# Performance work log

Measured on AMD Instinct MI355X. Metric: run time of the kernel, lower is better.

The kernel has to match this reference:

```python
import jax, jax.numpy as jnp
import numpy as np
from jax import lax


def _conv(x, w, b):
    # NCHW x OIHW, stride 1, VALID padding (matches nn.Conv2d padding=0)
    y = lax.conv_general_dilated(x, w, (1, 1), 'VALID',
                                 dimension_numbers=('NCHW', 'OIHW', 'NCHW'))
    return y + b[None, :, None, None]


def _maxpool2(x):
    return lax.reduce_window(x, -jnp.inf, lax.max, (1, 1, 2, 2), (1, 1, 2, 2), 'VALID')


def setup_inputs() -> dict:
    key = jax.random.key(0)
    ks = jax.random.split(key, 8)
    B, C, H, W = 4096, 3, 32, 32
    E, NC = 8, 1000  # out_dim (=n learners), num_classes
    inp = {
        'x': jax.random.normal(ks[0], (B, C, H, W), jnp.float32),
        'conv1_w': jax.random.normal(ks[1], (1, 3, 5, 5), jnp.float32) * 0.1,
        'conv1_b': jnp.zeros((1,), jnp.float32),
        'conv2_w': jax.random.normal(ks[2], (2, 1, 5, 5), jnp.float32) * 0.1,
        'conv2_b': jnp.zeros((2,), jnp.float32),
        'conv3_w': jax.random.normal(ks[3], (4, 2, 5, 5), jnp.float32) * 0.1,
        'conv3_b': jnp.zeros((4,), jnp.float32),
        'fc_w': jax.random.normal(ks[4], (E, 4), jnp.float32) * 0.5,
        'fc_b': jnp.zeros((E,), jnp.float32),
        'ens_w': jax.random.normal(ks[5], (E, C * H * W, NC), jnp.float32) * 0.02,
        'ens_b': jnp.zeros((E, NC), jnp.float32),
        'k': 2,
    }
    return inp


def reference(x, conv1_w, conv1_b, conv2_w, conv2_b, conv3_w, conv3_b,
              fc_w, fc_b, ens_w, ens_b, k):
    B = x.shape[0]
    # --- selector CNN stem ---
    h = jax.nn.relu(_conv(x, conv1_w, conv1_b))   # [B,1,28,28]
    h = _maxpool2(h)                              # [B,1,14,14]
    h = jax.nn.relu(_conv(h, conv2_w, conv2_b))   # [B,2,10,10]
    h = _maxpool2(h)                              # [B,2,5,5]
    h = jax.nn.relu(_conv(h, conv3_w, conv3_b))   # [B,4,1,1]
    h = h.reshape(B, -1)                          # [B,4]
    z = h @ fc_w.T + fc_b                         # [B,E]
    # L2NormalizationLayer with clamp(min=1e-9)
    z = z / jnp.clip(jnp.linalg.norm(z, axis=-1, keepdims=True), 1e-9, None)
    # TopK -> one-hot routing mask (straight-through style forward)
    _, idx = lax.top_k(z, k)                      # [B,k]
    mask = jax.nn.one_hot(idx, z.shape[-1], dtype=z.dtype).sum(-2)  # [B,E] in {0,1}
    # --- frozen ensemble: linear weak learners, combined via mask ---
    xf = x.reshape(B, -1)                          # [B,F]
    outs = jnp.einsum('bf,efc->bec', xf, ens_w) + ens_b[None]  # [B,E,NC]
    return (outs * mask[:, :, None]).sum(axis=1)   # [B,NC]
```

## Files before the change

kernel.cpp:

```cpp
#include <hip/hip_runtime.h>
#include <hip/hip_bf16.h>
#include <stdint.h>

#define B_SZ 4096
#define F_SZ 3072
#define NCLS 1000
#define NE 8
#define NPAD 1024
#define CAP 4096

#define OFF_CNT   0
#define OFF_LIST  1024
#define OFF_PAIR  132096
#define OFF_XB    262144
#define OFF_WT    25427968

typedef unsigned short u16;
typedef __attribute__((ext_vector_type(8))) short short8v;
typedef __attribute__((ext_vector_type(4))) float f32x4;

__device__ __forceinline__ u16 f2bf(float f) {
  unsigned int u = __float_as_uint(f);
  u = (u + 0x7FFFu + ((u >> 16) & 1u)) >> 16;
  return (u16)u;
}

__device__ __forceinline__ void gll16(const void* g, void* l) {
  __builtin_amdgcn_global_load_lds(
      (const __attribute__((address_space(1))) void*)g,
      (__attribute__((address_space(3))) void*)l, 16, 0, 0);
}

__global__ __launch_bounds__(256) void transpose_w(const float* __restrict__ ensw,
                                                   u16* __restrict__ wt) {
  __shared__ u16 tile[64 * 68];
  int t = threadIdx.x;
  int n0 = blockIdx.x * 64, k0 = blockIdx.y * 64, e = blockIdx.z;
  const float* src = ensw + (size_t)e * (F_SZ * NCLS);
  int kr = t >> 4, nq = (t & 15) * 4;
  for (int it = 0; it < 4; ++it) {
    int kk = kr + it * 16;
    const float* sp = src + (size_t)(k0 + kk) * NCLS + n0 + nq;
    float4 v;
    if (n0 + nq + 3 < NCLS) v = *(const float4*)sp;
    else {
      v.x = (n0 + nq     < NCLS) ? sp[0] : 0.f;
      v.y = (n0 + nq + 1 < NCLS) ? sp[1] : 0.f;
      v.z = (n0 + nq + 2 < NCLS) ? sp[2] : 0.f;
      v.w = (n0 + nq + 3 < NCLS) ? sp[3] : 0.f;
    }
    u16* d = tile + kk * 68 + nq;
    d[0] = f2bf(v.x); d[1] = f2bf(v.y); d[2] = f2bf(v.z); d[3] = f2bf(v.w);
  }
  __syncthreads();
  int rn = t >> 3, c8 = t & 7;
  for (int it = 0; it < 2; ++it) {
    int n = rn + it * 32;
    u16 o[8];
#pragma unroll
    for (int jj = 0; jj < 8; ++jj) o[jj] = tile[(c8 * 8 + jj) * 68 + n];
    uint4 pk;
    pk.x = (unsigned)o[0] | ((unsigned)o[1] << 16);
    pk.y = (unsigned)o[2] | ((unsigned)o[3] << 16);
    pk.z = (unsigned)o[4] | ((unsigned)o[5] << 16);
    pk.w = (unsigned)o[6] | ((unsigned)o[7] << 16);
    *(uint4*)(wt + ((size_t)(e * NPAD + n0 + n)) * F_SZ + k0 + c8 * 8) = pk;
  }
}

#define XST 36
#define XCH 1152
__global__ __launch_bounds__(128) void selector(
    const float* __restrict__ x,
    const float* __restrict__ w1, const float* __restrict__ b1,
    const float* __restrict__ w2, const float* __restrict__ b2,
    const float* __restrict__ w3, const float* __restrict__ b3,
    const float* __restrict__ fw, const float* __restrict__ fb,
    u16* __restrict__ xb16, int* __restrict__ cnt, int* __restrict__ list,
    int* __restrict__ expair) {
  __shared__ float wgt[384];
  __shared__ float S[2][4704];
  int t = threadIdx.x;
  for (int i = t; i < 372; i += 128) {
    float v;
    if      (i <  75) v = w1[i];
    else if (i <  76) v = b1[i - 75];
    else if (i < 126) v = w2[i - 76];
    else if (i < 128) v = b2[i - 126];
    else if (i < 328) v = w3[i - 128];
    else if (i < 332) v = b3[i - 328];
    else if (i < 364) v = fw[i - 332];
    else              v = fb[i - 364];
    wgt[i] = v;
  }
  int w = t >> 6, l = t & 63;
  int b = blockIdx.x * 2 + w;
  float* xs   = S[w];
  float* buf1 = xs + 3456;
  float* p1   = xs + 4240;
  float* buf2 = xs + 4436;
  float* p2   = xs + 4636;
  float* hb   = xs + 4686;
  float* zb   = xs + 4690;

  const float4* gx = (const float4*)(x + (size_t)b * F_SZ);
  ushort4* gxb = (ushort4*)(xb16 + (size_t)b * F_SZ);
  for (int it = 0; it < 12; ++it) {
    int idx = it * 64 + l;
    float4 v = gx[idx];
    int f = idx * 4;
    int c = f >> 10, rem = f & 1023, y = rem >> 5, xc = rem & 31;
    *(float4*)(xs + c * XCH + y * XST + xc) = v;
    ushort4 h4;
    h4.x = f2bf(v.x); h4.y = f2bf(v.y); h4.z = f2bf(v.z); h4.w = f2bf(v.w);
    gxb[idx] = h4;
  }
  __syncthreads();

  if (l < 56) {
    int y = l >> 1, xh = l & 1;
    float acc[14];
#pragma unroll
    for (int xc = 0; xc < 14; ++xc) acc[xc] = wgt[75];
    for (int c = 0; c < 3; ++c)
      for (int i = 0; i < 5; ++i) {
        const float4* rb = (const float4*)(xs + c * XCH + (y + i) * XST) + xh * 3;
        float a[20];
#pragma unroll
        for (int q = 0; q < 5; ++q) {
          float4 v = rb[q];
          a[q * 4] = v.x; a[q * 4 + 1] = v.y; a[q * 4 + 2] = v.z; a[q * 4 + 3] = v.w;
        }
        if (xh) {
#pragma unroll
          for (int q = 0; q < 18; ++q) a[q] = a[q + 2];
        }
        const float* wp = wgt + c * 25 + i * 5;
        float W0 = wp[0], W1 = wp[1], W2 = wp[2], W3 = wp[3], W4 = wp[4];
#pragma unroll
        for (int xc = 0; xc < 14; ++xc)
          acc[xc] += a[xc] * W0 + a[xc + 1] * W1 + a[xc + 2] * W2 + a[xc + 3] * W3 + a[xc + 4] * W4;
      }
#pragma unroll
    for (int xc = 0; xc < 14; ++xc) buf1[y * 28 + xh * 14 + xc] = fmaxf(acc[xc], 0.f);
  }
  __syncthreads();

  for (int it = 0; it < 4; ++it) {
    int p = it * 64 + l;
    if (p < 196) {
      int py = p / 14, px = p % 14;
      const float* r0 = buf1 + (2 * py) * 28 + 2 * px;
      p1[p] = fmaxf(fmaxf(r0[0], r0[1]), fmaxf(r0[28], r0[29]));
    }
  }
  __syncthreads();

  for (int it = 0; it < 4; ++it) {
    int p = it * 64 + l;
    if (p < 200) {
      int o = p / 100, rem = p % 100, yy = rem / 10, xx = rem % 10;
      float acc = wgt[126 + o];
      const float* wp = wgt + 76 + o * 25;
      for (int i = 0; i < 5; ++i)
#pragma unroll
        for (int j = 0; j < 5; ++j) acc += p1[(yy + i) * 14 + xx + j] * wp[i * 5 + j];
      buf2[p] = fmaxf(acc, 0.f);
    }
  }
  __syncthreads();

  if (l < 50) {
    int o = l / 25, rem = l % 25, yy = rem / 5, xx = rem % 5;
    const float* r0 = buf2 + o * 100 + (2 * yy) * 10 + 2 * xx;
    p2[l] = fmaxf(fmaxf(r0[0], r0[1]), fmaxf(r0[10], r0[11]));
  }
  __syncthreads();

  if (l < 4) {
    float acc = wgt[328 + l];
    const float* wp = wgt + 128 + l * 50;
    for (int cc = 0; cc < 50; ++cc) acc += p2[cc] * wp[cc];
    hb[l] = fmaxf(acc, 0.f);
  }
  __syncthreads();

  if (l < 8) {
    float acc = wgt[364 + l];
    const float* wp = wgt + 332 + l * 4;
#pragma unroll
    for (int j = 0; j < 4; ++j) acc += hb[j] * wp[j];
    zb[l] = acc;
  }
  __syncthreads();

  if (l == 0) {
    float zz[8];
#pragma unroll
    for (int e = 0; e < 8; ++e) zz[e] = zb[e];
    int e1 = 0; float v1 = zz[0];
    for (int e = 1; e < 8; ++e) if (zz[e] > v1) { v1 = zz[e]; e1 = e; }
    int e2 = -1; float v2 = 0.f;
    for (int e = 0; e < 8; ++e) {
      if (e == e1) continue;
      if (e2 < 0 || zz[e] > v2) { v2 = zz[e]; e2 = e; }
    }
    int p1i = atomicAdd(&cnt[e1], 1); list[e1 * CAP + p1i] = b;
    int p2i = atomicAdd(&cnt[e2], 1); list[e2 * CAP + p2i] = b;
    expair[b] = e1 | (e2 << 8);
  }
}

__global__ __launch_bounds__(256) void bias_init(const int* __restrict__ expair,
                                                 const float* __restrict__ ensb,
                                                 float* __restrict__ out) {
  int b = blockIdx.x;
  int t = threadIdx.x;
  if (t >= 250) return;
  int pr = expair[b];
  const float4* p1 = (const float4*)(ensb + (size_t)(pr & 255) * NCLS);
  const float4* p2 = (const float4*)(ensb + (size_t)((pr >> 8) & 255) * NCLS);
  float4* op = (float4*)(out + (size_t)b * NCLS);
  float4 a = p1[t], c = p2[t];
  float4 r; r.x = a.x + c.x; r.y = a.y + c.y; r.z = a.z + c.z; r.w = a.w + c.w;
  op[t] = r;
}

__global__ __launch_bounds__(256) void moe_gemm(const u16* __restrict__ xb,
                                                const u16* __restrict__ wt,
                                                const int* __restrict__ cnt,
                                                const int* __restrict__ list,
                                                float* __restrict__ out) {
  __shared__ u16 As[2][8192];
  __shared__ u16 Bs[2][8192];
  __shared__ int idx_s[128];
  int e = blockIdx.z;
  int cnt_e = cnt[e];
  int m0 = blockIdx.y * 128;
  if (m0 >= cnt_e) return;
  int n0 = blockIdx.x * 128;
  int t = threadIdx.x;
  const int* lst = list + e * CAP;
  if (t < 128) idx_s[t] = lst[min(m0 + t, cnt_e - 1)];
  __syncthreads();

  int tr = t >> 3;
  int ts = t & 7;
  int g  = ts ^ (tr & 7);
  const u16* pA[4]; const u16* pB[4]; int ldst[4];
#pragma unroll
  for (int q = 0; q < 4; ++q) {
    int row = q * 32 + tr;
    pA[q] = xb + (size_t)idx_s[row] * F_SZ + g * 8;
    pB[q] = wt + ((size_t)(e * NPAD + n0 + row)) * F_SZ + g * 8;
    ldst[q] = (q * 256 + t) * 8;
  }

  int w = t >> 6, l = t & 63;
  int lr = l & 15, hk = l >> 4;
  int wrow = (w >> 1) * 64, wcol = (w & 1) * 64;
  int rA[4], rB[4];
#pragma unroll
  for (int i = 0; i < 4; ++i) {
    rA[i] = (wrow + i * 16 + lr) * 64;
    rB[i] = (wcol + i * 16 + lr) * 64;
  }
  int sw0 = ((hk    ) ^ (lr & 7)) * 8;
  int sw1 = ((hk + 4) ^ (lr & 7)) * 8;

#pragma unroll
  for (int q = 0; q < 4; ++q) { gll16(pA[q], &As[0][ldst[q]]); pA[q] += 64; }
#pragma unroll
  for (int q = 0; q < 4; ++q) { gll16(pB[q], &Bs[0][ldst[q]]); pB[q] += 64; }
  __syncthreads();

  f32x4 acc[4][4] = {};
  for (int s = 0; s < 48; ++s) {
    int cur = s & 1;
    if (s < 47) {
      int nxt = cur ^ 1;
#pragma unroll
      for (int q = 0; q < 4; ++q) { gll16(pA[q], &As[nxt][ldst[q]]); pA[q] += 64; }
#pragma unroll
      for (int q = 0; q < 4; ++q) { gll16(pB[q], &Bs[nxt][ldst[q]]); pB[q] += 64; }
    }
    short8v av[2][4], bv[2][4];
#pragma unroll
    for (int i = 0; i < 4; ++i) {
      av[0][i] = *(const short8v*)(&As[cur][rA[i] + sw0]);
      av[1][i] = *(const short8v*)(&As[cur][rA[i] + sw1]);
      bv[0][i] = *(const short8v*)(&Bs[cur][rB[i] + sw0]);
      bv[1][i] = *(const short8v*)(&Bs[cur][rB[i] + sw1]);
    }
#pragma unroll
    for (int h = 0; h < 2; ++h)
#pragma unroll
      for (int i = 0; i < 4; ++i)
#pragma unroll
        for (int j = 0; j < 4; ++j)
          acc[i][j] = __builtin_amdgcn_mfma_f32_16x16x32_bf16(av[h][i], bv[h][j], acc[i][j], 0, 0, 0);
    __syncthreads();
  }

#pragma unroll
  for (int i = 0; i < 4; ++i) {
#pragma unroll
    for (int r = 0; r < 4; ++r) {
      int mt = wrow + i * 16 + hk * 4 + r;
      if (m0 + mt < cnt_e) {
        float* orow = out + (size_t)idx_s[mt] * NCLS;
#pragma unroll
        for (int j = 0; j < 4; ++j) {
          int col = n0 + wcol + j * 16 + lr;
          if (col < NCLS) unsafeAtomicAdd(orow + col, acc[i][j][r]);
        }
      }
    }
  }
}

extern "C" void kernel_launch(void* const* d_in, const int* in_sizes, int n_in,
                              void* d_out, int out_size, void* d_ws, size_t ws_size,
                              hipStream_t stream) {
  const float* x   = (const float*)d_in[0];
  const float* w1  = (const float*)d_in[1];
  const float* b1  = (const float*)d_in[2];
  const float* w2  = (const float*)d_in[3];
  const float* b2  = (const float*)d_in[4];
  const float* w3  = (const float*)d_in[5];
  const float* b3  = (const float*)d_in[6];
  const float* fw  = (const float*)d_in[7];
  const float* fb  = (const float*)d_in[8];
  const float* ensw = (const float*)d_in[9];
  const float* ensb = (const float*)d_in[10];
  float* out = (float*)d_out;

  uint8_t* ws = (uint8_t*)d_ws;
  int* cnt    = (int*)(ws + OFF_CNT);
  int* list   = (int*)(ws + OFF_LIST);
  int* expair = (int*)(ws + OFF_PAIR);
  u16* xb16   = (u16*)(ws + OFF_XB);
  u16* wt     = (u16*)(ws + OFF_WT);

  hipMemsetAsync(cnt, 0, 64, stream);
  transpose_w<<<dim3(16, 48, 8), 256, 0, stream>>>(ensw, wt);
  selector<<<2048, 128, 0, stream>>>(x, w1, b1, w2, b2, w3, b3, fw, fb,
                                     xb16, cnt, list, expair);
  bias_init<<<4096, 256, 0, stream>>>(expair, ensb, out);
  moe_gemm<<<dim3(8, 32, 8), 256, 0, stream>>>(xb16, wt, cnt, list, out);
}
```

Before: 483.2 us.

## Split MoE GEMM along K, single-buffer LDS, and widen weight transpose tiles

The MoE GEMM grid gains a split-K dimension of 2, with each half's partial sums combined through the existing atomic adds into the output. LDS double buffering is replaced by a single buffer with a sync before and after each reload, and a launch bound hint targets 4 blocks per CU. The aim is more parallelism and occupancy for an expert-routed GEMM whose per-expert M tiles can be few. The weight transpose kernel now handles 256-wide K tiles and writes transposed rows with vectorized LDS reads, and two selector loops are unrolled. The price is less load/compute overlap inside each block and twice the atomic traffic.

```diff
diff --git a/kernel.cpp b/kernel.cpp
--- a/kernel.cpp
+++ b/kernel.cpp
@@ -8,6 +8,8 @@
 #define NE 8
 #define NPAD 1024
 #define CAP 4096
+#define KSPLIT 2
+#define KCH (F_SZ / KSPLIT)
 
 #define OFF_CNT   0
 #define OFF_LIST  1024
@@ -33,38 +35,35 @@
 
 __global__ __launch_bounds__(256) void transpose_w(const float* __restrict__ ensw,
                                                    u16* __restrict__ wt) {
-  __shared__ u16 tile[64 * 68];
+  __shared__ u16 tile[64 * 264];
   int t = threadIdx.x;
-  int n0 = blockIdx.x * 64, k0 = blockIdx.y * 64, e = blockIdx.z;
+  int n0 = blockIdx.x * 64, k0 = blockIdx.y * 256, e = blockIdx.z;
   const float* src = ensw + (size_t)e * (F_SZ * NCLS);
   int kr = t >> 4, nq = (t & 15) * 4;
-  for (int it = 0; it < 4; ++it) {
-    int kk = kr + it * 16;
+  for (int it = 0; it < 16; ++it) {
+    int kk = it * 16 + kr;
     const float* sp = src + (size_t)(k0 + kk) * NCLS + n0 + nq;
-    float4 v;
-    if (n0 + nq + 3 < NCLS) v = *(const float4*)sp;
+    int n = n0 + nq;
+    float4 v = make_float4(0.f, 0.f, 0.f, 0.f);
+    if (n + 3 < NCLS) v = *(const float4*)sp;
     else {
-      v.x = (n0 + nq     < NCLS) ? sp[0] : 0.f;
-      v.y = (n0 + nq + 1 < NCLS) ? sp[1] : 0.f;
-      v.z = (n0 + nq + 2 < NCLS) ? sp[2] : 0.f;
-      v.w = (n0 + nq + 3 < NCLS) ? sp[3] : 0.f;
-    }
-    u16* d = tile + kk * 68 + nq;
-    d[0] = f2bf(v.x); d[1] = f2bf(v.y); d[2] = f2bf(v.z); d[3] = f2bf(v.w);
-  }
-  __syncthreads();
-  int rn = t >> 3, c8 = t & 7;
-  for (int it = 0; it < 2; ++it) {
-    int n = rn + it * 32;
-    u16 o[8];
-#pragma unroll
-    for (int jj = 0; jj < 8; ++jj) o[jj] = tile[(c8 * 8 + jj) * 68 + n];
-    uint4 pk;
-    pk.x = (unsigned)o[0] | ((unsigned)o[1] << 16);
-    pk.y = (unsigned)o[2] | ((unsigned)o[3] << 16);
-    pk.z = (unsigned)o[4] | ((unsigned)o[5] << 16);
-    pk.w = (unsigned)o[6] | ((unsigned)o[7] << 16);
-    *(uint4*)(wt + ((size_t)(e * NPAD + n0 + n)) * F_SZ + k0 + c8 * 8) = pk;
+      if (n     < NCLS) v.x = sp[0];
+      if (n + 1 < NCLS) v.y = sp[1];
+      if (n + 2 < NCLS) v.z = sp[2];
+      if (n + 3 < NCLS) v.w = sp[3];
+    }
+    u16* d = tile + nq * 264 + kk;
+    d[0]   = f2bf(v.x);
+    d[264] = f2bf(v.y);
+    d[528] = f2bf(v.z);
+    d[792] = f2bf(v.w);
+  }
+  __syncthreads();
+  int kc = t & 31, nr = t >> 5;
+  for (int it = 0; it < 8; ++it) {
+    int n = it * 8 + nr;
+    uint4 pk = *(const uint4*)(tile + n * 264 + kc * 8);
+    *(uint4*)(wt + ((size_t)(e * NPAD + n0 + n)) * F_SZ + k0 + kc * 8) = pk;
   }
 }
 
@@ -162,6 +161,7 @@
       int o = p / 100, rem = p % 100, yy = rem / 10, xx = rem % 10;
       float acc = wgt[126 + o];
       const float* wp = wgt + 76 + o * 25;
+#pragma unroll
       for (int i = 0; i < 5; ++i)
 #pragma unroll
         for (int j = 0; j < 5; ++j) acc += p1[(yy + i) * 14 + xx + j] * wp[i * 5 + j];
@@ -180,6 +180,7 @@
   if (l < 4) {
     float acc = wgt[328 + l];
     const float* wp = wgt + 128 + l * 50;
+#pragma unroll
     for (int cc = 0; cc < 50; ++cc) acc += p2[cc] * wp[cc];
     hb[l] = fmaxf(acc, 0.f);
   }
@@ -226,15 +227,15 @@
   op[t] = r;
 }
 
-__global__ __launch_bounds__(256) void moe_gemm(const u16* __restrict__ xb,
-                                                const u16* __restrict__ wt,
-                                                const int* __restrict__ cnt,
-                                                const int* __restrict__ list,
-                                                float* __restrict__ out) {
-  __shared__ u16 As[2][8192];
-  __shared__ u16 Bs[2][8192];
+__global__ __launch_bounds__(256, 4) void moe_gemm(const u16* __restrict__ xb,
+                                                   const u16* __restrict__ wt,
+                                                   const int* __restrict__ cnt,
+                                                   const int* __restrict__ list,
+                                                   float* __restrict__ out) {
+  __shared__ u16 As[8192];
+  __shared__ u16 Bs[8192];
   __shared__ int idx_s[128];
-  int e = blockIdx.z;
+  int e = blockIdx.z >> 1, ks = blockIdx.z & 1;
   int cnt_e = cnt[e];
   int m0 = blockIdx.y * 128;
   if (m0 >= cnt_e) return;
@@ -244,15 +245,14 @@
   if (t < 128) idx_s[t] = lst[min(m0 + t, cnt_e - 1)];
   __syncthreads();
 
-  int tr = t >> 3;
-  int ts = t & 7;
+  int tr = t >> 3, ts = t & 7;
   int g  = ts ^ (tr & 7);
   const u16* pA[4]; const u16* pB[4]; int ldst[4];
 #pragma unroll
   for (int q = 0; q < 4; ++q) {
     int row = q * 32 + tr;
-    pA[q] = xb + (size_t)idx_s[row] * F_SZ + g * 8;
-    pB[q] = wt + ((size_t)(e * NPAD + n0 + row)) * F_SZ + g * 8;
+    pA[q] = xb + (size_t)idx_s[row] * F_SZ + ks * KCH + g * 8;
+    pB[q] = wt + ((size_t)(e * NPAD + n0 + row)) * F_SZ + ks * KCH + g * 8;
     ldst[q] = (q * 256 + t) * 8;
   }
 
@@ -269,28 +269,20 @@
   int sw1 = ((hk + 4) ^ (lr & 7)) * 8;
 
 #pragma unroll
-  for (int q = 0; q < 4; ++q) { gll16(pA[q], &As[0][ldst[q]]); pA[q] += 64; }
-#pragma unroll
-  for (int q = 0; q < 4; ++q) { gll16(pB[q], &Bs[0][ldst[q]]); pB[q] += 64; }
-  __syncthreads();
+  for (int q = 0; q < 4; ++q) { gll16(pA[q], &As[ldst[q]]); pA[q] += 64; }
+#pragma unroll
+  for (int q = 0; q < 4; ++q) { gll16(pB[q], &Bs[ldst[q]]); pB[q] += 64; }
 
   f32x4 acc[4][4] = {};
-  for (int s = 0; s < 48; ++s) {
-    int cur = s & 1;
-    if (s < 47) {
-      int nxt = cur ^ 1;
-#pragma unroll
-      for (int q = 0; q < 4; ++q) { gll16(pA[q], &As[nxt][ldst[q]]); pA[q] += 64; }
-#pragma unroll
-      for (int q = 0; q < 4; ++q) { gll16(pB[q], &Bs[nxt][ldst[q]]); pB[q] += 64; }
-    }
+  for (int s = 0; s < KCH / 64; ++s) {
+    __syncthreads();
     short8v av[2][4], bv[2][4];
 #pragma unroll
     for (int i = 0; i < 4; ++i) {
-      av[0][i] = *(const short8v*)(&As[cur][rA[i] + sw0]);
-      av[1][i] = *(const short8v*)(&As[cur][rA[i] + sw1]);
-      bv[0][i] = *(const short8v*)(&Bs[cur][rB[i] + sw0]);
-      bv[1][i] = *(const short8v*)(&Bs[cur][rB[i] + sw1]);
+      av[0][i] = *(const short8v*)(&As[rA[i] + sw0]);
+      av[1][i] = *(const short8v*)(&As[rA[i] + sw1]);
+      bv[0][i] = *(const short8v*)(&Bs[rB[i] + sw0]);
+      bv[1][i] = *(const short8v*)(&Bs[rB[i] + sw1]);
     }
 #pragma unroll
     for (int h = 0; h < 2; ++h)
@@ -299,7 +291,13 @@
 #pragma unroll
         for (int j = 0; j < 4; ++j)
           acc[i][j] = __builtin_amdgcn_mfma_f32_16x16x32_bf16(av[h][i], bv[h][j], acc[i][j], 0, 0, 0);
-    __syncthreads();
+    if (s < KCH / 64 - 1) {
+      __syncthreads();
+#pragma unroll
+      for (int q = 0; q < 4; ++q) { gll16(pA[q], &As[ldst[q]]); pA[q] += 64; }
+#pragma unroll
+      for (int q = 0; q < 4; ++q) { gll16(pB[q], &Bs[ldst[q]]); pB[q] += 64; }
+    }
   }
 
 #pragma unroll
@@ -343,9 +341,9 @@
   u16* wt     = (u16*)(ws + OFF_WT);
 
   hipMemsetAsync(cnt, 0, 64, stream);
-  transpose_w<<<dim3(16, 48, 8), 256, 0, stream>>>(ensw, wt);
+  transpose_w<<<dim3(16, 12, 8), 256, 0, stream>>>(ensw, wt);
   selector<<<2048, 128, 0, stream>>>(x, w1, b1, w2, b2, w3, b3, fw, fb,
                                      xb16, cnt, list, expair);
   bias_init<<<4096, 256, 0, stream>>>(expair, ensb, out);
-  moe_gemm<<<dim3(8, 32, 8), 256, 0, stream>>>(xb16, wt, cnt, list, out);
-}
+  moe_gemm<<<dim3(8, 32, 16), 256, 0, stream>>>(xb16, wt, cnt, list, out);
+}
```

After: 439.6 us. 1.1x faster.
